# Performance work log

Measured on AMD Instinct MI355X. Metric: run time of the kernel, lower is better.

Reference implementation:

```python
import jax, jax.numpy as jnp
import numpy as np

D_MODEL = 1024
N_HEADS = 16
D_K = 64
D_V = 64
NEG = -1000000000.0

def setup_inputs() -> dict:
    key = jax.random.key(0)
    ks = jax.random.split(key, 10)
    B, L = 2, 2048
    inp = {
        'q': jax.random.normal(ks[0], (B, L, D_MODEL), jnp.float32),
        'k': jax.random.normal(ks[1], (B, L, D_MODEL), jnp.float32),
        'v': jax.random.normal(ks[2], (B, L, D_MODEL), jnp.float32),
        'mask': jnp.ones((B, L), jnp.float32),
        'Wq': jax.random.normal(ks[3], (N_HEADS * D_K, D_MODEL), jnp.float32) * 0.02,
        'Wk': jax.random.normal(ks[4], (N_HEADS * D_K, D_MODEL), jnp.float32) * 0.02,
        'Wv': jax.random.normal(ks[5], (N_HEADS * D_V, D_MODEL), jnp.float32) * 0.02,
        'Wo': jax.random.normal(ks[6], (D_MODEL, N_HEADS * D_V), jnp.float32) * 0.02,
        'scaling_factor': jnp.array(1.0, jnp.float32),
        'tau': jnp.array(1.0, jnp.float32),
        'ln_w': jnp.ones((D_MODEL,), jnp.float32),
        'ln_b': jnp.zeros((D_MODEL,), jnp.float32),
        'window_size': 1024,
        'n_heads': N_HEADS,
    }
    return inp


def reference(q, k, v, mask, Wq, Wk, Wv, Wo, scaling_factor, tau, ln_w, ln_b, window_size, n_heads):
    B, L, dm = q.shape
    H = n_heads
    dk = Wq.shape[0] // H
    dv = Wv.shape[0] // H
    # projections: nn.Linear(x) = x @ W.T, then split heads -> (B,H,L,d)
    Q = jnp.einsum('bld,hkd->bhlk', q, Wq.reshape(H, dk, dm))
    K = jnp.einsum('bld,hkd->bhlk', k, Wk.reshape(H, dk, dm))
    V = jnp.einsum('bld,hkd->bhlk', v, Wv.reshape(H, dv, dm))
    scores = jnp.einsum('bhlk,bhmk->bhlm', Q, K) / jnp.sqrt(jnp.float32(dk))
    idx = jnp.arange(L)
    rel = idx[:, None] - idx[None, :]                      # (L,L) q_idx - kv_idx
    wmask = (jnp.abs(rel) <= window_size // 2).astype(jnp.float32)
    # input mask (B,L) applies along the QUERY dim per original expand semantics
    combined = mask[:, None, :, None] * wmask[None, None]  # (B,1,L,L)
    scores = jnp.where(combined == 0, NEG, scores)
    bias = jnp.exp(-jnp.abs(rel.astype(jnp.float32) / scaling_factor) / tau)
    scores = scores - bias[None, None]
    attention = jax.nn.softmax(scores, axis=-1)            # (B,H,L,L)
    out = jnp.einsum('bhlm,bhmd->bhld', attention, V)
    out = out.transpose(0, 2, 1, 3).reshape(B, L, H * dv)
    out = out @ Wo.T
    # residual + LayerNorm(eps=1e-6)
    x = out + q
    mu = jnp.mean(x, axis=-1, keepdims=True)
    var = jnp.var(x, axis=-1, keepdims=True)
    x = (x - mu) / jnp.sqrt(var + 1e-6) * ln_w + ln_b
    return (x, attention)
```

## Files before the change

kernel.cpp:

```cpp
#include <hip/hip_runtime.h>
#include <hip/hip_bf16.h>
#include <cstddef>

#define L_SEQ 2048
#define BATCH 2
#define HEADS 16
#define DMODEL 1024
#define DHEAD 64
#define ROWS (BATCH * L_SEQ)
#define X_ELEMS ((size_t)ROWS * DMODEL)
#define ATT_OFF X_ELEMS

#define TQ 64
#define TKEY 32

typedef __attribute__((ext_vector_type(8))) short bf16x8;
typedef __attribute__((ext_vector_type(4))) float f32x4;
typedef __attribute__((ext_vector_type(8))) unsigned short u16x8;

template<bool BF>
__device__ __forceinline__ float ldin(const void* p, size_t i) {
    if constexpr (BF) return __bfloat162float(((const __hip_bfloat16*)p)[i]);
    else              return ((const float*)p)[i];
}
template<bool BF>
__device__ __forceinline__ void stout(void* p, size_t i, float v) {
    if constexpr (BF) ((__hip_bfloat16*)p)[i] = __float2bfloat16(v);
    else              ((float*)p)[i] = v;
}

__device__ __forceinline__ float bf2f(unsigned short u) {
    return __uint_as_float(((unsigned)u) << 16);
}
__device__ __forceinline__ unsigned short f2bf(float f) {
    __hip_bfloat16 h = __float2bfloat16(f);
    return *reinterpret_cast<unsigned short*>(&h);
}
template<bool BF>
__device__ __forceinline__ float4 ld4g(const void* p, size_t i) {
    if constexpr (BF) {
        const ushort4 u = *reinterpret_cast<const ushort4*>((const unsigned short*)p + i);
        return make_float4(bf2f(u.x), bf2f(u.y), bf2f(u.z), bf2f(u.w));
    } else {
        return *reinterpret_cast<const float4*>((const float*)p + i);
    }
}
template<bool BF>
__device__ __forceinline__ void st4g(void* p, size_t i, float4 v) {
    if constexpr (BF) {
        ushort4 u; u.x = f2bf(v.x); u.y = f2bf(v.y); u.z = f2bf(v.z); u.w = f2bf(v.w);
        *reinterpret_cast<ushort4*>((unsigned short*)p + i) = u;
    } else {
        *reinterpret_cast<float4*>((float*)p + i) = v;
    }
}

__global__ void detect_kernel(const void* mask, int* flag) {
    unsigned u = *(const unsigned*)mask;
    flag[0] = (u == 0x3F803F80u) ? 1 : 0;
    flag[1] = 0;
}

template<bool XBF, bool WBF, int SA, int SB>
__global__ __launch_bounds__(256)
void gemm_mfma(const void* __restrict__ X, const void* __restrict__ W,
               float* __restrict__ C, const int* __restrict__ flag,
               int bfexp, int mode)
{
    if (((*flag) != 0) != (bfexp != 0)) return;
    __shared__ short Ahi[128 * 40];
    __shared__ short Alo[(SA > 1) ? 128 * 40 : 8];
    __shared__ short Bhi[64 * 40];
    __shared__ short Blo[(SB > 1) ? 64 * 40 : 8];
    const int t = threadIdx.x;
    const int n0 = blockIdx.x * 64;
    const int m0 = blockIdx.y * 128;
    const int w = t >> 6, lid = t & 63;
    const int wr = w >> 1, wc = w & 1;
    const int lrow = lid & 15, lk = lid >> 4;

    f32x4 acc[4][2];
    #pragma unroll
    for (int i = 0; i < 4; ++i)
        #pragma unroll
        for (int j = 0; j < 2; ++j) acc[i][j] = (f32x4){0.f, 0.f, 0.f, 0.f};

    float4 rx[4], rw[2];
    auto loadX = [&](int k0) {
        #pragma unroll
        for (int i = 0; i < 4; ++i) {
            const int slot = t + i * 256;
            const int row = slot >> 3, c4 = slot & 7;
            rx[i] = ld4g<XBF>(X, (size_t)(m0 + row) * DMODEL + k0 + c4 * 4);
        }
    };
    auto loadW = [&](int k0) {
        #pragma unroll
        for (int i = 0; i < 2; ++i) {
            const int slot = t + i * 256;
            const int row = slot >> 3, c4 = slot & 7;
            rw[i] = ld4g<WBF>(W, (size_t)(n0 + row) * DMODEL + k0 + c4 * 4);
        }
    };

    loadX(0); loadW(0);
    for (int k0 = 0; k0 < DMODEL; k0 += 32) {
        __syncthreads();
        #pragma unroll
        for (int i = 0; i < 4; ++i) {
            const int slot = t + i * 256;
            const int row = slot >> 3, c4 = slot & 7;
            const int base = row * 40 + c4 * 4;
            const float f[4] = {rx[i].x, rx[i].y, rx[i].z, rx[i].w};
            unsigned short hs[4], ls[4];
            #pragma unroll
            for (int e = 0; e < 4; ++e) {
                hs[e] = f2bf(f[e]);
                if constexpr (SA > 1) ls[e] = f2bf(f[e] - bf2f(hs[e]));
            }
            *(ushort4*)&Ahi[base] = make_ushort4(hs[0], hs[1], hs[2], hs[3]);
            if constexpr (SA > 1)
                *(ushort4*)&Alo[base] = make_ushort4(ls[0], ls[1], ls[2], ls[3]);
        }
        #pragma unroll
        for (int i = 0; i < 2; ++i) {
            const int slot = t + i * 256;
            const int row = slot >> 3, c4 = slot & 7;
            const int base = row * 40 + c4 * 4;
            const float f[4] = {rw[i].x, rw[i].y, rw[i].z, rw[i].w};
            unsigned short hs[4], ls[4];
            #pragma unroll
            for (int e = 0; e < 4; ++e) {
                hs[e] = f2bf(f[e]);
                if constexpr (SB > 1) ls[e] = f2bf(f[e] - bf2f(hs[e]));
            }
            *(ushort4*)&Bhi[base] = make_ushort4(hs[0], hs[1], hs[2], hs[3]);
            if constexpr (SB > 1)
                *(ushort4*)&Blo[base] = make_ushort4(ls[0], ls[1], ls[2], ls[3]);
        }
        __syncthreads();
        if (k0 + 32 < DMODEL) { loadX(k0 + 32); loadW(k0 + 32); }

        bf16x8 ah[4], al[4], bh[2], bl[2];
        #pragma unroll
        for (int mi = 0; mi < 4; ++mi) {
            const int r = wr * 64 + mi * 16 + lrow;
            ah[mi] = *(const bf16x8*)&Ahi[r * 40 + lk * 8];
            if constexpr (SA > 1) al[mi] = *(const bf16x8*)&Alo[r * 40 + lk * 8];
        }
        #pragma unroll
        for (int ni = 0; ni < 2; ++ni) {
            const int r = wc * 32 + ni * 16 + lrow;
            bh[ni] = *(const bf16x8*)&Bhi[r * 40 + lk * 8];
            if constexpr (SB > 1) bl[ni] = *(const bf16x8*)&Blo[r * 40 + lk * 8];
        }
        #pragma unroll
        for (int mi = 0; mi < 4; ++mi)
            #pragma unroll
            for (int ni = 0; ni < 2; ++ni) {
                acc[mi][ni] = __builtin_amdgcn_mfma_f32_16x16x32_bf16(ah[mi], bh[ni], acc[mi][ni], 0, 0, 0);
                if constexpr (SA > 1)
                    acc[mi][ni] = __builtin_amdgcn_mfma_f32_16x16x32_bf16(al[mi], bh[ni], acc[mi][ni], 0, 0, 0);
                if constexpr (SB > 1)
                    acc[mi][ni] = __builtin_amdgcn_mfma_f32_16x16x32_bf16(ah[mi], bl[ni], acc[mi][ni], 0, 0, 0);
            }
    }
    #pragma unroll
    for (int mi = 0; mi < 4; ++mi)
        #pragma unroll
        for (int ni = 0; ni < 2; ++ni)
            #pragma unroll
            for (int r = 0; r < 4; ++r) {
                const int grow = m0 + wr * 64 + mi * 16 + lk * 4 + r;
                const int gcol = n0 + wc * 32 + ni * 16 + lrow;
                const float v = acc[mi][ni][r];
                if (mode == 0) {
                    const int bb = grow >> 11, l = grow & (L_SEQ - 1);
                    const int hh = gcol >> 6,  d = gcol & 63;
                    C[(((size_t)bb * HEADS + hh) * L_SEQ + l) * DHEAD + d] = v;
                } else if (mode == 2) {
                    const int bb = grow >> 11, l = grow & (L_SEQ - 1);
                    const int hh = gcol >> 6,  d = gcol & 63;
                    ((unsigned short*)C)[(((size_t)bb * HEADS + hh) * L_SEQ + l) * DHEAD + d] = f2bf(v);
                } else {
                    C[(size_t)grow * DMODEL + gcol] = v;
                }
            }
}

template<bool XBF, bool WBF>
__global__ void gemm_check(const void* __restrict__ X, const void* __restrict__ W,
                           const float* __restrict__ C, const int* __restrict__ flag,
                           int bfexp, int* __restrict__ bad)
{
    if (((*flag) != 0) != (bfexp != 0)) return;
    const int t = threadIdx.x;
    const int m = (t * 16 + 5) & (ROWS - 1);
    const int n = (t * 67 + 1) & (DMODEL - 1);
    float ref = 0.f;
    for (int k = 0; k < DMODEL; ++k)
        ref += ldin<XBF>(X, (size_t)m * DMODEL + k) * ldin<WBF>(W, (size_t)n * DMODEL + k);
    const int bb = m >> 11, l = m & (L_SEQ - 1);
    const int hh = n >> 6,  d = n & 63;
    const float got = C[(((size_t)bb * HEADS + hh) * L_SEQ + l) * DHEAD + d];
    if (fabsf(got - ref) > 0.03f) atomicOr(bad, 1);
}

template<bool XBF, bool WBF>
__global__ __launch_bounds__(256)
void gemm_tile(const void* __restrict__ X, const void* __restrict__ W,
               float* __restrict__ C, const int* __restrict__ flag,
               int bfexp, int mode, const int* __restrict__ bad)
{
    if (((*flag) != 0) != (bfexp != 0)) return;
    if (*bad == 0) return;
    __shared__ float Xs[16][132];
    __shared__ float Ws[16][68];
    const int t  = threadIdx.x;
    const int tx = t & 15, ty = t >> 4;
    const int n0 = blockIdx.x * 64;
    const int m0 = blockIdx.y * 128;
    float acc[8][4] = {};
    float4 rx[2], rw;

    auto loadX = [&](int k0) {
        #pragma unroll
        for (int i = 0; i < 2; ++i) {
            const int slot = t + i * 256;
            const int row = slot >> 2, c4 = slot & 3;
            rx[i] = ld4g<XBF>(X, (size_t)(m0 + row) * DMODEL + k0 + c4 * 4);
        }
    };
    auto loadW = [&](int k0) {
        const int row = t >> 2, c4 = t & 3;
        rw = ld4g<WBF>(W, (size_t)(n0 + row) * DMODEL + k0 + c4 * 4);
    };

    loadX(0); loadW(0);
    for (int k0 = 0; k0 < DMODEL; k0 += 16) {
        __syncthreads();
        #pragma unroll
        for (int i = 0; i < 2; ++i) {
            const int slot = t + i * 256;
            const int row = slot >> 2, c4 = slot & 3;
            Xs[c4*4+0][row] = rx[i].x; Xs[c4*4+1][row] = rx[i].y;
            Xs[c4*4+2][row] = rx[i].z; Xs[c4*4+3][row] = rx[i].w;
        }
        {
            const int row = t >> 2, c4 = t & 3;
            Ws[c4*4+0][row] = rw.x; Ws[c4*4+1][row] = rw.y;
            Ws[c4*4+2][row] = rw.z; Ws[c4*4+3][row] = rw.w;
        }
        __syncthreads();
        if (k0 + 16 < DMODEL) { loadX(k0 + 16); loadW(k0 + 16); }
        #pragma unroll
        for (int kk = 0; kk < 16; ++kk) {
            const float4 a0 = *(const float4*)&Xs[kk][ty*8];
            const float4 a1 = *(const float4*)&Xs[kk][ty*8+4];
            const float4 b0 = *(const float4*)&Ws[kk][tx*4];
            const float am[8] = {a0.x,a0.y,a0.z,a0.w,a1.x,a1.y,a1.z,a1.w};
            const float bn[4] = {b0.x,b0.y,b0.z,b0.w};
            #pragma unroll
            for (int ii = 0; ii < 8; ++ii)
                #pragma unroll
                for (int jj = 0; jj < 4; ++jj)
                    acc[ii][jj] += am[ii] * bn[jj];
        }
    }
    const int nb = n0 + tx * 4;
    #pragma unroll
    for (int ii = 0; ii < 8; ++ii) {
        const int m = m0 + ty * 8 + ii;
        const float4 v = make_float4(acc[ii][0], acc[ii][1], acc[ii][2], acc[ii][3]);
        if (mode == 0) {
            const int bb = m >> 11, l = m & (L_SEQ - 1);
            const int hh = nb >> 6, d = nb & 63;
            *(float4*)&C[(((size_t)bb * HEADS + hh) * L_SEQ + l) * DHEAD + d] = v;
        } else if (mode == 2) {
            const int bb = m >> 11, l = m & (L_SEQ - 1);
            const int hh = nb >> 6, d = nb & 63;
            ushort4 u; u.x = f2bf(v.x); u.y = f2bf(v.y); u.z = f2bf(v.z); u.w = f2bf(v.w);
            *(ushort4*)&((unsigned short*)C)[(((size_t)bb * HEADS + hh) * L_SEQ + l) * DHEAD + d] = u;
        } else {
            *(float4*)&C[(size_t)m * DMODEL + nb] = v;
        }
    }
}

template<bool BF>
__global__ __launch_bounds__(256, 4)
void attn_mfma(const float* __restrict__ Qb, const unsigned short* __restrict__ Kb16,
               const unsigned short* __restrict__ Vb16, const void* __restrict__ mask,
               const void* __restrict__ sfp, const void* __restrict__ taup,
               const int* __restrict__ wszp, float* __restrict__ Ob,
               void* __restrict__ out, const int* __restrict__ flag, int bfexp)
{
    if (((*flag) != 0) != (bfexp != 0)) return;
    const int qb = blockIdx.x;
    const int bh = blockIdx.y;
    const int b  = bh >> 4, h = bh & 15;
    const int t  = threadIdx.x;
    const int lid = t & 63;
    const int w   = t >> 6;
    const int wq0 = w * 16;
    const int lrow = lid & 15, lgrp = lid >> 4;
    const int qt0 = qb * TQ;

    __shared__ float tab[1152];
    __shared__ unsigned short Klds[TKEY * 72];
    __shared__ unsigned short Vt[DHEAD * 40];
    __shared__ unsigned short Plds[TQ * 40];
    __shared__ float mscratch[2560];
    __shared__ int   mflags[TQ];

    const float sfv  = ldin<BF>(sfp, 0);
    const float tauv = ldin<BF>(taup, 0);
    const int   W2   = (*wszp) >> 1;
    const float cb   = -1.0f / (tauv * fabsf(sfv));

    for (int i = t; i < 1152; i += 256) tab[i] = __expf(cb * (float)i);

    bf16x8 qhi0, qlo0, qhi1, qlo1;
    {
        const size_t qoff = ((size_t)bh * L_SEQ + qt0 + wq0 + lrow) * DHEAD;
        const float4 a0 = *(const float4*)&Qb[qoff + lgrp * 8];
        const float4 a1 = *(const float4*)&Qb[qoff + lgrp * 8 + 4];
        const float4 a2 = *(const float4*)&Qb[qoff + 32 + lgrp * 8];
        const float4 a3 = *(const float4*)&Qb[qoff + 32 + lgrp * 8 + 4];
        const float f0[8] = {a0.x,a0.y,a0.z,a0.w,a1.x,a1.y,a1.z,a1.w};
        const float f1[8] = {a2.x,a2.y,a2.z,a2.w,a3.x,a3.y,a3.z,a3.w};
        #pragma unroll
        for (int e = 0; e < 8; ++e) {
            const unsigned short h0 = f2bf(f0[e]);
            const unsigned short h1 = f2bf(f1[e]);
            qhi0[e] = (short)h0; qlo0[e] = (short)f2bf(f0[e] - bf2f(h0));
            qhi1[e] = (short)h1; qlo1[e] = (short)f2bf(f1[e] - bf2f(h1));
        }
    }

    int jlo0 = qt0 - W2;            if (jlo0 < 0) jlo0 = 0;
    int jhi0 = qt0 + TQ - 1 + W2;   if (jhi0 > L_SEQ - 1) jhi0 = L_SEQ - 1;
    const int NT = (jhi0 - jlo0 + TKEY) / TKEY;

    const size_t kvbase = (size_t)bh * L_SEQ * DHEAD;
    u16x8 stgK, stgV;
    auto issueK = [&](int j0) {
        int jr = j0 + (t >> 3); if (jr > L_SEQ - 1) jr = L_SEQ - 1;
        stgK = *(const u16x8*)&Kb16[kvbase + (size_t)jr * DHEAD + (t & 7) * 8];
    };
    auto issueV = [&](int j0) {
        int jr = j0 + (t & 31); if (jr > L_SEQ - 1) jr = L_SEQ - 1;
        stgV = *(const u16x8*)&Vb16[kvbase + (size_t)jr * DHEAD + (t >> 5) * 8];
    };

    float racc[4] = {0.f, 0.f, 0.f, 0.f};
    issueK(jlo0);
    for (int kt = 0; kt < NT; ++kt) {
        __syncthreads();
        *(u16x8*)&Klds[(t >> 3) * 72 + (t & 7) * 8] = stgK;
        __syncthreads();
        if (kt + 1 < NT) issueK(jlo0 + (kt + 1) * TKEY);
        const int jt0 = jlo0 + kt * TKEY;
        #pragma unroll
        for (int jt = 0; jt < 2; ++jt) {
            const bf16x8 kb0 = *(const bf16x8*)&Klds[(jt * 16 + lrow) * 72 + lgrp * 8];
            const bf16x8 kb1 = *(const bf16x8*)&Klds[(jt * 16 + lrow) * 72 + 32 + lgrp * 8];
            f32x4 s = (f32x4){0.f, 0.f, 0.f, 0.f};
            s = __builtin_amdgcn_mfma_f32_16x16x32_bf16(qhi0, kb0, s, 0, 0, 0);
            s = __builtin_amdgcn_mfma_f32_16x16x32_bf16(qhi1, kb1, s, 0, 0, 0);
            s = __builtin_amdgcn_mfma_f32_16x16x32_bf16(qlo0, kb0, s, 0, 0, 0);
            s = __builtin_amdgcn_mfma_f32_16x16x32_bf16(qlo1, kb1, s, 0, 0, 0);
            const int j = jt0 + jt * 16 + lrow;
            #pragma unroll
            for (int r = 0; r < 4; ++r) {
                const int q = qt0 + wq0 + lgrp * 4 + r;
                int arel = q - j; arel = arel < 0 ? -arel : arel;
                const int ai = arel < 1151 ? arel : 1151;
                const float sc = s[r] * 0.125f - tab[ai];
                racc[r] += (arel <= W2) ? __expf(sc) : 0.f;
            }
        }
    }
    #pragma unroll
    for (int r = 0; r < 4; ++r) {
        racc[r] += __shfl_xor(racc[r], 1);
        racc[r] += __shfl_xor(racc[r], 2);
        racc[r] += __shfl_xor(racc[r], 4);
        racc[r] += __shfl_xor(racc[r], 8);
        racc[r] = 1.0f / racc[r];
    }

    f32x4 o[4];
    #pragma unroll
    for (int df = 0; df < 4; ++df) o[df] = (f32x4){0.f, 0.f, 0.f, 0.f};

    issueK(jlo0); issueV(jlo0);
    for (int kt = 0; kt < NT; ++kt) {
        __syncthreads();
        *(u16x8*)&Klds[(t >> 3) * 72 + (t & 7) * 8] = stgK;
        {
            const int jv = t & 31, d0v = (t >> 5) * 8;
            #pragma unroll
            for (int e = 0; e < 8; ++e)
                Vt[(d0v + e) * 40 + jv] = (unsigned short)stgV[e];
        }
        __syncthreads();
        if (kt + 1 < NT) { issueK(jlo0 + (kt + 1) * TKEY); issueV(jlo0 + (kt + 1) * TKEY); }
        const int jt0 = jlo0 + kt * TKEY;
        #pragma unroll
        for (int jt = 0; jt < 2; ++jt) {
            const bf16x8 kb0 = *(const bf16x8*)&Klds[(jt * 16 + lrow) * 72 + lgrp * 8];
            const bf16x8 kb1 = *(const bf16x8*)&Klds[(jt * 16 + lrow) * 72 + 32 + lgrp * 8];
            f32x4 s = (f32x4){0.f, 0.f, 0.f, 0.f};
            s = __builtin_amdgcn_mfma_f32_16x16x32_bf16(qhi0, kb0, s, 0, 0, 0);
            s = __builtin_amdgcn_mfma_f32_16x16x32_bf16(qhi1, kb1, s, 0, 0, 0);
            s = __builtin_amdgcn_mfma_f32_16x16x32_bf16(qlo0, kb0, s, 0, 0, 0);
            s = __builtin_amdgcn_mfma_f32_16x16x32_bf16(qlo1, kb1, s, 0, 0, 0);
            const int j = jt0 + jt * 16 + lrow;
            #pragma unroll
            for (int r = 0; r < 4; ++r) {
                const int q = qt0 + wq0 + lgrp * 4 + r;
                int arel = q - j; arel = arel < 0 ? -arel : arel;
                const int ai = arel < 1151 ? arel : 1151;
                const float sc = s[r] * 0.125f - tab[ai];
                const float p = (arel <= W2) ? __expf(sc) * racc[r] : 0.f;
                Plds[(wq0 + lgrp * 4 + r) * 40 + jt * 16 + lrow] = f2bf(p);
            }
        }
        __syncthreads();
        const bf16x8 pA = *(const bf16x8*)&Plds[(wq0 + lrow) * 40 + lgrp * 8];
        #pragma unroll
        for (int df = 0; df < 4; ++df) {
            const bf16x8 vB = *(const bf16x8*)&Vt[(df * 16 + lrow) * 40 + lgrp * 8];
            o[df] = __builtin_amdgcn_mfma_f32_16x16x32_bf16(pA, vB, o[df], 0, 0, 0);
        }
        {
            const int rloc = wq0 + (lid >> 2);
            const int c0 = (lid & 3) * 8;
            const u16x8 pv = *(const u16x8*)&Plds[rloc * 40 + c0];
            const size_t abase = ATT_OFF + ((size_t)bh * L_SEQ + qt0 + rloc) * (size_t)L_SEQ + jt0 + c0;
            st4g<BF>(out, abase,     make_float4(bf2f(pv[0]), bf2f(pv[1]), bf2f(pv[2]), bf2f(pv[3])));
            st4g<BF>(out, abase + 4, make_float4(bf2f(pv[4]), bf2f(pv[5]), bf2f(pv[6]), bf2f(pv[7])));
        }
    }

    #pragma unroll
    for (int df = 0; df < 4; ++df)
        #pragma unroll
        for (int r = 0; r < 4; ++r) {
            const int q = qt0 + wq0 + lgrp * 4 + r;
            Ob[((size_t)b * L_SEQ + q) * DMODEL + h * DHEAD + df * 16 + lrow] = o[df][r];
        }

    const int jend = jlo0 + NT * TKEY;
    const float4 z4 = make_float4(0.f, 0.f, 0.f, 0.f);
    const int lw4 = jlo0 >> 2;
    for (int s = t; s < TQ * lw4; s += 256) {
        const int r = s / lw4, c = (s - r * lw4) * 4;
        st4g<BF>(out, ATT_OFF + ((size_t)bh * L_SEQ + qt0 + r) * (size_t)L_SEQ + c, z4);
    }
    const int rw4 = (L_SEQ - jend) >> 2;
    for (int s = t; s < TQ * rw4; s += 256) {
        const int r = s / rw4, c = jend + (s - r * rw4) * 4;
        st4g<BF>(out, ATT_OFF + ((size_t)bh * L_SEQ + qt0 + r) * (size_t)L_SEQ + c, z4);
    }

    if (t < TQ) {
        const float mv = ldin<BF>(mask, (size_t)b * L_SEQ + qt0 + t);
        mflags[t] = (mv == 0.0f) ? 1 : 0;
    }
    __syncthreads();
    int any = 0;
    #pragma unroll 1
    for (int r = 0; r < TQ; ++r) any |= mflags[r];
    if (any) {
        float* Pbuf  = &mscratch[0];
        float* redm  = &mscratch[2048];
        float* partm = &mscratch[2304];
        for (int r = 0; r < TQ; ++r) {
            if (!mflags[r]) continue;
            const int q = qt0 + r;
            const size_t abase = ATT_OFF + ((size_t)bh * L_SEQ + q) * (size_t)L_SEQ;
            float lsum = 0.f;
            for (int c = t; c < L_SEQ; c += 256) {
                int arel = q - c; arel = arel < 0 ? -arel : arel;
                const float p = __expf(-__expf(cb * (float)arel));
                Pbuf[c] = p; lsum += p;
            }
            redm[t] = lsum; __syncthreads();
            for (int o2 = 128; o2 > 0; o2 >>= 1) { if (t < o2) redm[t] += redm[t + o2]; __syncthreads(); }
            const float inv = 1.0f / redm[0];
            for (int c = t; c < L_SEQ; c += 256) stout<BF>(out, abase + c, Pbuf[c] * inv);
            const int g = t >> 6, d = t & 63;
            float acc = 0.f;
            for (int c = g; c < L_SEQ; c += 4)
                acc += Pbuf[c] * bf2f(Vb16[kvbase + (size_t)c * DHEAD + d]);
            partm[t] = acc; __syncthreads();
            if (t < DHEAD) {
                const float o4 = (partm[t] + partm[DHEAD + t] + partm[2*DHEAD + t] + partm[3*DHEAD + t]) * inv;
                Ob[((size_t)b * L_SEQ + q) * DMODEL + h * DHEAD + t] = o4;
            }
            __syncthreads();
        }
    }
}

template<bool BF>
__global__ __launch_bounds__(256)
void ln_kernel(const float* __restrict__ Pb, const void* __restrict__ qin,
               const void* __restrict__ lnw, const void* __restrict__ lnb,
               void* __restrict__ out, const int* __restrict__ flag, int bfexp) {
    if (((*flag) != 0) != (bfexp != 0)) return;
    const int row = blockIdx.x;
    const int t = threadIdx.x;
    __shared__ float xs[DMODEL];
    __shared__ float red[256];
    float s = 0.f;
    for (int i = t; i < DMODEL; i += 256) {
        const float v = Pb[(size_t)row * DMODEL + i] + ldin<BF>(qin, (size_t)row * DMODEL + i);
        xs[i] = v; s += v;
    }
    red[t] = s; __syncthreads();
    for (int o = 128; o > 0; o >>= 1) { if (t < o) red[t] += red[t + o]; __syncthreads(); }
    const float mu = red[0] * (1.0f / DMODEL);
    __syncthreads();
    float s2 = 0.f;
    for (int i = t; i < DMODEL; i += 256) { const float dv = xs[i] - mu; s2 += dv * dv; }
    red[t] = s2; __syncthreads();
    for (int o = 128; o > 0; o >>= 1) { if (t < o) red[t] += red[t + o]; __syncthreads(); }
    const float rstd = rsqrtf(red[0] * (1.0f / DMODEL) + 1e-6f);
    for (int i = t; i < DMODEL; i += 256) {
        const float y = (xs[i] - mu) * rstd * ldin<BF>(lnw, i) + ldin<BF>(lnb, i);
        stout<BF>(out, (size_t)row * DMODEL + i, y);
    }
}

extern "C" void kernel_launch(void* const* d_in, const int* in_sizes, int n_in,
                              void* d_out, int out_size, void* d_ws, size_t ws_size,
                              hipStream_t stream) {
    const void* q_in = d_in[0];
    const void* k_in = d_in[1];
    const void* v_in = d_in[2];
    const void* mask = d_in[3];
    const void* Wq   = d_in[4];
    const void* Wk   = d_in[5];
    const void* Wv   = d_in[6];
    const void* Wo   = d_in[7];
    const void* sf   = d_in[8];
    const void* tau  = d_in[9];
    const void* lnw  = d_in[10];
    const void* lnb  = d_in[11];
    const int*  wsz  = (const int*)d_in[12];
    (void)in_sizes; (void)n_in; (void)out_size; (void)ws_size;

    int*   flag = (int*)d_ws;
    int*   bad  = flag + 1;
    float* A    = ((float*)d_ws) + 64;
    float* Qb   = A;
    float* Kb   = A + 4194304;
    float* Vb   = A + 8388608;
    float* Ob   = A + 12582912;
    float* Pb   = A;

    detect_kernel<<<1, 1, 0, stream>>>(mask, flag);

    dim3 gm(DMODEL / 64, ROWS / 128);

    gemm_mfma<false, false, 2, 2><<<gm, 256, 0, stream>>>(q_in, Wq, Qb, flag, 0, 0);
    gemm_mfma<true,  true,  1, 1><<<gm, 256, 0, stream>>>(q_in, Wq, Qb, flag, 1, 0);
    gemm_mfma<false, false, 2, 2><<<gm, 256, 0, stream>>>(k_in, Wk, Kb, flag, 0, 2);
    gemm_mfma<true,  true,  1, 1><<<gm, 256, 0, stream>>>(k_in, Wk, Kb, flag, 1, 2);
    gemm_mfma<false, false, 2, 2><<<gm, 256, 0, stream>>>(v_in, Wv, Vb, flag, 0, 2);
    gemm_mfma<true,  true,  1, 1><<<gm, 256, 0, stream>>>(v_in, Wv, Vb, flag, 1, 2);

    gemm_check<false, false><<<1, 256, 0, stream>>>(q_in, Wq, Qb, flag, 0, bad);
    gemm_check<true,  true ><<<1, 256, 0, stream>>>(q_in, Wq, Qb, flag, 1, bad);
    gemm_tile<false, false><<<gm, 256, 0, stream>>>(q_in, Wq, Qb, flag, 0, 0, bad);
    gemm_tile<true,  true ><<<gm, 256, 0, stream>>>(q_in, Wq, Qb, flag, 1, 0, bad);
    gemm_tile<false, false><<<gm, 256, 0, stream>>>(k_in, Wk, Kb, flag, 0, 2, bad);
    gemm_tile<true,  true ><<<gm, 256, 0, stream>>>(k_in, Wk, Kb, flag, 1, 2, bad);
    gemm_tile<false, false><<<gm, 256, 0, stream>>>(v_in, Wv, Vb, flag, 0, 2, bad);
    gemm_tile<true,  true ><<<gm, 256, 0, stream>>>(v_in, Wv, Vb, flag, 1, 2, bad);

    dim3 ag(L_SEQ / TQ, BATCH * HEADS);
    attn_mfma<false><<<ag, 256, 0, stream>>>(Qb, (const unsigned short*)Kb,
                                             (const unsigned short*)Vb, mask, sf, tau, wsz,
                                             Ob, d_out, flag, 0);
    attn_mfma<true ><<<ag, 256, 0, stream>>>(Qb, (const unsigned short*)Kb,
                                             (const unsigned short*)Vb, mask, sf, tau, wsz,
                                             Ob, d_out, flag, 1);

    gemm_mfma<false, false, 2, 2><<<gm, 256, 0, stream>>>(Ob, Wo, Pb, flag, 0, 1);
    gemm_mfma<false, true,  2, 1><<<gm, 256, 0, stream>>>(Ob, Wo, Pb, flag, 1, 1);
    gemm_tile<false, false><<<gm, 256, 0, stream>>>(Ob, Wo, Pb, flag, 0, 1, bad);
    gemm_tile<false, true ><<<gm, 256, 0, stream>>>(Ob, Wo, Pb, flag, 1, 1, bad);

    ln_kernel<false><<<ROWS, 256, 0, stream>>>(Pb, q_in, lnw, lnb, d_out, flag, 0);
    ln_kernel<true ><<<ROWS, 256, 0, stream>>>(Pb, q_in, lnw, lnb, d_out, flag, 1);
}
```

Baseline: 947.7 us.

## Pre-split inputs and weights into bf16 hi/lo planes for split-precision GEMMs

Adds a conversion kernel that splits the fp32 activations and weights once into bf16 high and low planes in workspace. A new 128x128-tile MFMA GEMM then consumes these planes directly with three bf16 MFMAs per tile (hi*hi, lo*hi, hi*lo). This replaces the earlier per-tile in-kernel splitting for the QKV and output projections. The aim is to move conversion work out of the GEMM inner loop and enlarge the N tile for more reuse, at the cost of extra memory traffic for the split buffers and a larger workspace requirement. It falls back to the old path if the workspace is too small.

```diff
diff --git a/kernel.cpp b/kernel.cpp
--- a/kernel.cpp
+++ b/kernel.cpp
@@ -59,6 +59,139 @@
     unsigned u = *(const unsigned*)mask;
     flag[0] = (u == 0x3F803F80u) ? 1 : 0;
     flag[1] = 0;
+}
+
+__global__ __launch_bounds__(256)
+void conv_split(const void* s0, const void* s1, const void* s2, const void* s3,
+                unsigned short* h0, unsigned short* h1, unsigned short* h2, unsigned short* h3,
+                unsigned short* l0, unsigned short* l1, unsigned short* l2, unsigned short* l3,
+                size_t nelem, const int* __restrict__ flag, int force_fp32)
+{
+    const int z = blockIdx.z;
+    const void* src = (z == 0) ? s0 : (z == 1) ? s1 : (z == 2) ? s2 : s3;
+    unsigned short* hd = (z == 0) ? h0 : (z == 1) ? h1 : (z == 2) ? h2 : h3;
+    unsigned short* ld = (z == 0) ? l0 : (z == 1) ? l1 : (z == 2) ? l2 : l3;
+    const int isbf = force_fp32 ? 0 : (*flag);
+    const size_t i0 = ((size_t)blockIdx.x * 256 + threadIdx.x) * 8;
+    const size_t stride = (size_t)gridDim.x * 256 * 8;
+    for (size_t i = i0; i < nelem; i += stride) {
+        u16x8 hv, lv;
+        if (isbf) {
+            hv = *(const u16x8*)((const unsigned short*)src + i);
+            #pragma unroll
+            for (int e = 0; e < 8; ++e) lv[e] = 0;
+        } else {
+            const float4 a = *(const float4*)((const float*)src + i);
+            const float4 b = *(const float4*)((const float*)src + i + 4);
+            const float f[8] = {a.x, a.y, a.z, a.w, b.x, b.y, b.z, b.w};
+            #pragma unroll
+            for (int e = 0; e < 8; ++e) {
+                const unsigned short h = f2bf(f[e]);
+                hv[e] = h;
+                lv[e] = f2bf(f[e] - bf2f(h));
+            }
+        }
+        *(u16x8*)(hd + i) = hv;
+        *(u16x8*)(ld + i) = lv;
+    }
+}
+
+__global__ __launch_bounds__(256)
+void gemm_ps(const unsigned short* __restrict__ Xh, const unsigned short* __restrict__ Xl,
+             const unsigned short* __restrict__ Wh, const unsigned short* __restrict__ Wl,
+             float* __restrict__ C, int mode)
+{
+    __shared__ short Ah[128 * 40];
+    __shared__ short Al[128 * 40];
+    __shared__ short Bh[128 * 40];
+    __shared__ short Bl[128 * 40];
+    const int t = threadIdx.x;
+    const int n0 = blockIdx.x * 128;
+    const int m0 = blockIdx.y * 128;
+    const int w = t >> 6, lid = t & 63;
+    const int wr = w >> 1, wc = w & 1;
+    const int lrow = lid & 15, lk = lid >> 4;
+
+    f32x4 acc[4][4];
+    #pragma unroll
+    for (int i = 0; i < 4; ++i)
+        #pragma unroll
+        for (int j = 0; j < 4; ++j) acc[i][j] = (f32x4){0.f, 0.f, 0.f, 0.f};
+
+    u16x8 rAh[2], rAl[2], rBh[2], rBl[2];
+    auto loadAll = [&](int k0) {
+        #pragma unroll
+        for (int i = 0; i < 2; ++i) {
+            const int slot = i * 256 + t;
+            const int row = slot >> 2, c8 = slot & 3;
+            const size_t offA = (size_t)(m0 + row) * DMODEL + k0 + c8 * 8;
+            const size_t offB = (size_t)(n0 + row) * DMODEL + k0 + c8 * 8;
+            rAh[i] = *(const u16x8*)&Xh[offA];
+            rAl[i] = *(const u16x8*)&Xl[offA];
+            rBh[i] = *(const u16x8*)&Wh[offB];
+            rBl[i] = *(const u16x8*)&Wl[offB];
+        }
+    };
+
+    loadAll(0);
+    for (int k0 = 0; k0 < DMODEL; k0 += 32) {
+        __syncthreads();
+        #pragma unroll
+        for (int i = 0; i < 2; ++i) {
+            const int slot = i * 256 + t;
+            const int row = slot >> 2, c8 = slot & 3;
+            const int base = row * 40 + c8 * 8;
+            *(u16x8*)&Ah[base] = rAh[i];
+            *(u16x8*)&Al[base] = rAl[i];
+            *(u16x8*)&Bh[base] = rBh[i];
+            *(u16x8*)&Bl[base] = rBl[i];
+        }
+        __syncthreads();
+        if (k0 + 32 < DMODEL) loadAll(k0 + 32);
+
+        bf16x8 ah[4], al[4], bh[4], bl[4];
+        #pragma unroll
+        for (int mi = 0; mi < 4; ++mi) {
+            const int r = wr * 64 + mi * 16 + lrow;
+            ah[mi] = *(const bf16x8*)&Ah[r * 40 + lk * 8];
+            al[mi] = *(const bf16x8*)&Al[r * 40 + lk * 8];
+        }
+        #pragma unroll
+        for (int ni = 0; ni < 4; ++ni) {
+            const int r = wc * 64 + ni * 16 + lrow;
+            bh[ni] = *(const bf16x8*)&Bh[r * 40 + lk * 8];
+            bl[ni] = *(const bf16x8*)&Bl[r * 40 + lk * 8];
+        }
+        #pragma unroll
+        for (int mi = 0; mi < 4; ++mi)
+            #pragma unroll
+            for (int ni = 0; ni < 4; ++ni) {
+                acc[mi][ni] = __builtin_amdgcn_mfma_f32_16x16x32_bf16(ah[mi], bh[ni], acc[mi][ni], 0, 0, 0);
+                acc[mi][ni] = __builtin_amdgcn_mfma_f32_16x16x32_bf16(al[mi], bh[ni], acc[mi][ni], 0, 0, 0);
+                acc[mi][ni] = __builtin_amdgcn_mfma_f32_16x16x32_bf16(ah[mi], bl[ni], acc[mi][ni], 0, 0, 0);
+            }
+    }
+    #pragma unroll
+    for (int mi = 0; mi < 4; ++mi)
+        #pragma unroll
+        for (int ni = 0; ni < 4; ++ni)
+            #pragma unroll
+            for (int r = 0; r < 4; ++r) {
+                const int grow = m0 + wr * 64 + mi * 16 + lk * 4 + r;
+                const int gcol = n0 + wc * 64 + ni * 16 + lrow;
+                const float v = acc[mi][ni][r];
+                if (mode == 0) {
+                    const int bb = grow >> 11, l = grow & (L_SEQ - 1);
+                    const int hh = gcol >> 6,  d = gcol & 63;
+                    C[(((size_t)bb * HEADS + hh) * L_SEQ + l) * DHEAD + d] = v;
+                } else if (mode == 2) {
+                    const int bb = grow >> 11, l = grow & (L_SEQ - 1);
+                    const int hh = gcol >> 6,  d = gcol & 63;
+                    ((unsigned short*)C)[(((size_t)bb * HEADS + hh) * L_SEQ + l) * DHEAD + d] = f2bf(v);
+                } else {
+                    C[(size_t)grow * DMODEL + gcol] = v;
+                }
+            }
 }
 
 template<bool XBF, bool WBF, int SA, int SB>
@@ -551,50 +684,113 @@
     const void* lnw  = d_in[10];
     const void* lnb  = d_in[11];
     const int*  wsz  = (const int*)d_in[12];
-    (void)in_sizes; (void)n_in; (void)out_size; (void)ws_size;
+    (void)in_sizes; (void)n_in; (void)out_size;
 
     int*   flag = (int*)d_ws;
     int*   bad  = flag + 1;
     float* A    = ((float*)d_ws) + 64;
-    float* Qb   = A;
-    float* Kb   = A + 4194304;
-    float* Vb   = A + 8388608;
-    float* Ob   = A + 12582912;
-    float* Pb   = A;
 
     detect_kernel<<<1, 1, 0, stream>>>(mask, flag);
 
-    dim3 gm(DMODEL / 64, ROWS / 128);
-
-    gemm_mfma<false, false, 2, 2><<<gm, 256, 0, stream>>>(q_in, Wq, Qb, flag, 0, 0);
-    gemm_mfma<true,  true,  1, 1><<<gm, 256, 0, stream>>>(q_in, Wq, Qb, flag, 1, 0);
-    gemm_mfma<false, false, 2, 2><<<gm, 256, 0, stream>>>(k_in, Wk, Kb, flag, 0, 2);
-    gemm_mfma<true,  true,  1, 1><<<gm, 256, 0, stream>>>(k_in, Wk, Kb, flag, 1, 2);
-    gemm_mfma<false, false, 2, 2><<<gm, 256, 0, stream>>>(v_in, Wv, Vb, flag, 0, 2);
-    gemm_mfma<true,  true,  1, 1><<<gm, 256, 0, stream>>>(v_in, Wv, Vb, flag, 1, 2);
-
-    gemm_check<false, false><<<1, 256, 0, stream>>>(q_in, Wq, Qb, flag, 0, bad);
-    gemm_check<true,  true ><<<1, 256, 0, stream>>>(q_in, Wq, Qb, flag, 1, bad);
-    gemm_tile<false, false><<<gm, 256, 0, stream>>>(q_in, Wq, Qb, flag, 0, 0, bad);
-    gemm_tile<true,  true ><<<gm, 256, 0, stream>>>(q_in, Wq, Qb, flag, 1, 0, bad);
-    gemm_tile<false, false><<<gm, 256, 0, stream>>>(k_in, Wk, Kb, flag, 0, 2, bad);
-    gemm_tile<true,  true ><<<gm, 256, 0, stream>>>(k_in, Wk, Kb, flag, 1, 2, bad);
-    gemm_tile<false, false><<<gm, 256, 0, stream>>>(v_in, Wv, Vb, flag, 0, 2, bad);
-    gemm_tile<true,  true ><<<gm, 256, 0, stream>>>(v_in, Wv, Vb, flag, 1, 2, bad);
-
-    dim3 ag(L_SEQ / TQ, BATCH * HEADS);
-    attn_mfma<false><<<ag, 256, 0, stream>>>(Qb, (const unsigned short*)Kb,
-                                             (const unsigned short*)Vb, mask, sf, tau, wsz,
-                                             Ob, d_out, flag, 0);
-    attn_mfma<true ><<<ag, 256, 0, stream>>>(Qb, (const unsigned short*)Kb,
-                                             (const unsigned short*)Vb, mask, sf, tau, wsz,
-                                             Ob, d_out, flag, 1);
-
-    gemm_mfma<false, false, 2, 2><<<gm, 256, 0, stream>>>(Ob, Wo, Pb, flag, 0, 1);
-    gemm_mfma<false, true,  2, 1><<<gm, 256, 0, stream>>>(Ob, Wo, Pb, flag, 1, 1);
-    gemm_tile<false, false><<<gm, 256, 0, stream>>>(Ob, Wo, Pb, flag, 0, 1, bad);
-    gemm_tile<false, true ><<<gm, 256, 0, stream>>>(Ob, Wo, Pb, flag, 1, 1, bad);
-
-    ln_kernel<false><<<ROWS, 256, 0, stream>>>(Pb, q_in, lnw, lnb, d_out, flag, 0);
-    ln_kernel<true ><<<ROWS, 256, 0, stream>>>(Pb, q_in, lnw, lnb, d_out, flag, 1);
-}
+    const size_t NEED = ((size_t)29360128 + 64) * 4;
+    const bool presplit = (ws_size == 0) || (ws_size >= NEED);
+
+    dim3 agrid(L_SEQ / TQ, BATCH * HEADS);
+
+    if (presplit) {
+        unsigned short* XQh = (unsigned short*)(A);
+        unsigned short* XQl = XQh + 4194304;
+        unsigned short* XKh = (unsigned short*)(A + 4194304);
+        unsigned short* XKl = XKh + 4194304;
+        unsigned short* XVh = (unsigned short*)(A + 8388608);
+        unsigned short* XVl = XVh + 4194304;
+        unsigned short* WQh = (unsigned short*)(A + 12582912);
+        unsigned short* WQl = WQh + 1048576;
+        unsigned short* WKh = (unsigned short*)(A + 13631488);
+        unsigned short* WKl = WKh + 1048576;
+        unsigned short* WVh = (unsigned short*)(A + 14680064);
+        unsigned short* WVl = WVh + 1048576;
+        unsigned short* WOh = (unsigned short*)(A + 15728640);
+        unsigned short* WOl = WOh + 1048576;
+        float* Qb = A + 16777216;
+        float* Kb = A + 20971520;
+        float* Vb = A + 23068672;
+        float* Ob = A + 25165824;
+        unsigned short* XOh = (unsigned short*)(A);
+        unsigned short* XOl = XOh + 4194304;
+        float* Pb = A + 4194304;
+
+        conv_split<<<dim3(2048, 1, 3), 256, 0, stream>>>(
+            q_in, k_in, v_in, nullptr, XQh, XKh, XVh, nullptr, XQl, XKl, XVl, nullptr,
+            (size_t)ROWS * DMODEL, flag, 0);
+        conv_split<<<dim3(512, 1, 4), 256, 0, stream>>>(
+            Wq, Wk, Wv, Wo, WQh, WKh, WVh, WOh, WQl, WKl, WVl, WOl,
+            (size_t)DMODEL * DMODEL, flag, 0);
+
+        dim3 gp(DMODEL / 128, ROWS / 128);
+        gemm_ps<<<gp, 256, 0, stream>>>(XQh, XQl, WQh, WQl, Qb, 0);
+        gemm_ps<<<gp, 256, 0, stream>>>(XKh, XKl, WKh, WKl, Kb, 2);
+        gemm_ps<<<gp, 256, 0, stream>>>(XVh, XVl, WVh, WVl, Vb, 2);
+
+        dim3 gf(DMODEL / 64, ROWS / 128);
+        gemm_check<false, false><<<1, 256, 0, stream>>>(q_in, Wq, Qb, flag, 0, bad);
+        gemm_check<true,  true ><<<1, 256, 0, stream>>>(q_in, Wq, Qb, flag, 1, bad);
+        gemm_tile<false, false><<<gf, 256, 0, stream>>>(q_in, Wq, Qb, flag, 0, 0, bad);
+        gemm_tile<true,  true ><<<gf, 256, 0, stream>>>(q_in, Wq, Qb, flag, 1, 0, bad);
+        gemm_tile<false, false><<<gf, 256, 0, stream>>>(k_in, Wk, Kb, flag, 0, 2, bad);
+        gemm_tile<true,  true ><<<gf, 256, 0, stream>>>(k_in, Wk, Kb, flag, 1, 2, bad);
+        gemm_tile<false, false><<<gf, 256, 0, stream>>>(v_in, Wv, Vb, flag, 0, 2, bad);
+        gemm_tile<true,  true ><<<gf, 256, 0, stream>>>(v_in, Wv, Vb, flag, 1, 2, bad);
+
+        attn_mfma<false><<<agrid, 256, 0, stream>>>(Qb, (const unsigned short*)Kb,
+            (const unsigned short*)Vb, mask, sf, tau, wsz, Ob, d_out, flag, 0);
+        attn_mfma<true ><<<agrid, 256, 0, stream>>>(Qb, (const unsigned short*)Kb,
+            (const unsigned short*)Vb, mask, sf, tau, wsz, Ob, d_out, flag, 1);
+
+        conv_split<<<dim3(2048, 1, 1), 256, 0, stream>>>(
+            Ob, nullptr, nullptr, nullptr, XOh, nullptr, nullptr, nullptr,
+            XOl, nullptr, nullptr, nullptr, (size_t)ROWS * DMODEL, flag, 1);
+        gemm_ps<<<gp, 256, 0, stream>>>(XOh, XOl, WOh, WOl, Pb, 1);
+        gemm_tile<false, false><<<gf, 256, 0, stream>>>(Ob, Wo, Pb, flag, 0, 1, bad);
+        gemm_tile<false, true ><<<gf, 256, 0, stream>>>(Ob, Wo, Pb, flag, 1, 1, bad);
+
+        ln_kernel<false><<<ROWS, 256, 0, stream>>>(Pb, q_in, lnw, lnb, d_out, flag, 0);
+        ln_kernel<true ><<<ROWS, 256, 0, stream>>>(Pb, q_in, lnw, lnb, d_out, flag, 1);
+    } else {
+        float* Qb = A;
+        float* Kb = A + 4194304;
+        float* Vb = A + 8388608;
+        float* Ob = A + 12582912;
+        float* Pb = A;
+
+        dim3 gm(DMODEL / 64, ROWS / 128);
+        gemm_mfma<false, false, 2, 2><<<gm, 256, 0, stream>>>(q_in, Wq, Qb, flag, 0, 0);
+        gemm_mfma<true,  true,  1, 1><<<gm, 256, 0, stream>>>(q_in, Wq, Qb, flag, 1, 0);
+        gemm_mfma<false, false, 2, 2><<<gm, 256, 0, stream>>>(k_in, Wk, Kb, flag, 0, 2);
+        gemm_mfma<true,  true,  1, 1><<<gm, 256, 0, stream>>>(k_in, Wk, Kb, flag, 1, 2);
+        gemm_mfma<false, false, 2, 2><<<gm, 256, 0, stream>>>(v_in, Wv, Vb, flag, 0, 2);
+        gemm_mfma<true,  true,  1, 1><<<gm, 256, 0, stream>>>(v_in, Wv, Vb, flag, 1, 2);
+
+        gemm_check<false, false><<<1, 256, 0, stream>>>(q_in, Wq, Qb, flag, 0, bad);
+        gemm_check<true,  true ><<<1, 256, 0, stream>>>(q_in, Wq, Qb, flag, 1, bad);
+        gemm_tile<false, false><<<gm, 256, 0, stream>>>(q_in, Wq, Qb, flag, 0, 0, bad);
+        gemm_tile<true,  true ><<<gm, 256, 0, stream>>>(q_in, Wq, Qb, flag, 1, 0, bad);
+        gemm_tile<false, false><<<gm, 256, 0, stream>>>(k_in, Wk, Kb, flag, 0, 2, bad);
+        gemm_tile<true,  true ><<<gm, 256, 0, stream>>>(k_in, Wk, Kb, flag, 1, 2, bad);
+        gemm_tile<false, false><<<gm, 256, 0, stream>>>(v_in, Wv, Vb, flag, 0, 2, bad);
+        gemm_tile<true,  true ><<<gm, 256, 0, stream>>>(v_in, Wv, Vb, flag, 1, 2, bad);
+
+        attn_mfma<false><<<agrid, 256, 0, stream>>>(Qb, (const unsigned short*)Kb,
+            (const unsigned short*)Vb, mask, sf, tau, wsz, Ob, d_out, flag, 0);
+        attn_mfma<true ><<<agrid, 256, 0, stream>>>(Qb, (const unsigned short*)Kb,
+            (const unsigned short*)Vb, mask, sf, tau, wsz, Ob, d_out, flag, 1);
+
+        gemm_mfma<false, false, 2, 2><<<gm, 256, 0, stream>>>(Ob, Wo, Pb, flag, 0, 1);
+        gemm_mfma<false, true,  2, 1><<<gm, 256, 0, stream>>>(Ob, Wo, Pb, flag, 1, 1);
+        gemm_tile<false, false><<<gm, 256, 0, stream>>>(Ob, Wo, Pb, flag, 0, 1, bad);
+        gemm_tile<false, true ><<<gm, 256, 0, stream>>>(Ob, Wo, Pb, flag, 1, 1, bad);
+
+        ln_kernel<false><<<ROWS, 256, 0, stream>>>(Pb, q_in, lnw, lnb, d_out, flag, 0);
+        ln_kernel<true ><<<ROWS, 256, 0, stream>>>(Pb, q_in, lnw, lnb, d_out, flag, 1);
+    }
+}
```

Result: slower. 978.1 us (+3.2%).
